# Performance work log

Measured on AMD Instinct MI355X. Metric: run time of the kernel, lower is better.

Reference implementation:

```python
import jax, jax.numpy as jnp
import numpy as np


def setup_inputs() -> dict:
    key = jax.random.key(0)
    k1, k2, k3 = jax.random.split(key, 3)
    N, D, V = 16384, 256, 8192
    return {
        "z_real": jax.random.normal(k1, (N, D), jnp.float32),
        "z_imag": jax.random.normal(k2, (N, D), jnp.float32),
        "weight": jax.random.normal(k3, (V, 2 * D), jnp.float32) / np.sqrt(2 * D).astype(np.float32),
    }


def reference(z_real, z_imag, weight):
    sg = jax.lax.stop_gradient
    N, D = z_real.shape
    V = weight.shape[0]
    z_flat = jnp.concatenate([z_real, z_imag], axis=-1)  # (N, 2D)
    # Squared euclidean distance expansion; argmin over squared dist == argmin over cdist.
    x2 = jnp.sum(z_flat * z_flat, axis=-1, keepdims=True)            # (N, 1)
    w2 = jnp.sum(weight * weight, axis=-1)                           # (V,)
    d2 = x2 + w2[None, :] - 2.0 * jnp.einsum('nd,vd->nv', z_flat, weight)  # (N, V)
    indices = jnp.argmin(d2, axis=-1)                                # (N,)
    z_q = weight[indices]                                            # (N, 2D)
    # codebook loss + 0.25 * commitment loss, per-sample mean over feature dim
    loss_sample = jnp.mean((z_q - sg(z_flat)) ** 2, axis=-1) \
                + 0.25 * jnp.mean((sg(z_q) - z_flat) ** 2, axis=-1)  # (N,)
    # straight-through estimator
    z_q_st = z_flat + sg(z_q - z_flat)                               # (N, 2D)
    # entropy of empirical code usage (equivalent to one_hot(indices).mean(0))
    counts = jnp.zeros((V,), z_flat.dtype).at[indices].add(1.0)
    avg_probs = counts / jnp.asarray(N, z_flat.dtype)
    entropy = -jnp.sum(avg_probs * jnp.log(avg_probs + 1e-10))
    # split straight-through output back into real / imag halves (complex output)
    return z_q_st[..., :D], z_q_st[..., D:], loss_sample, indices, entropy
```

## Files before the change

### kernel.cpp

```cpp
#include <hip/hip_runtime.h>
#include <cmath>

typedef _Float16 half8 __attribute__((ext_vector_type(8)));
typedef float f32x4 __attribute__((ext_vector_type(4)));

constexpr int N = 16384;
constexpr int D = 256;
constexpr int K = 512;
constexpr int V = 8192;
constexpr float TAU = 0.015f;

#define GLOAD16(g, l) __builtin_amdgcn_global_load_lds(                     \
    (const __attribute__((address_space(1))) void*)(g),                    \
    (__attribute__((address_space(3))) void*)(l), 16, 0, 0)

__global__ __launch_bounds__(256) void vq_cvt_z(
    const float* __restrict__ zr, const float* __restrict__ zi,
    _Float16* __restrict__ Zf) {
  int t = blockIdx.x * 256 + threadIdx.x;
  int n = t >> 6, c8 = t & 63, k = c8 * 8;
  const float* src = (k < D) ? zr + (size_t)n * D + k : zi + (size_t)n * D + (k - D);
  float4 a = *(const float4*)src;
  float4 b = *(const float4*)(src + 4);
  half8 h;
  h[0] = (_Float16)a.x; h[1] = (_Float16)a.y; h[2] = (_Float16)a.z; h[3] = (_Float16)a.w;
  h[4] = (_Float16)b.x; h[5] = (_Float16)b.y; h[6] = (_Float16)b.z; h[7] = (_Float16)b.w;
  *(half8*)&Zf[(size_t)n * K + k] = h;
}

__global__ __launch_bounds__(256) void vq_cvt_w(
    const float* __restrict__ w, _Float16* __restrict__ Wf) {
  int t = blockIdx.x * 256 + threadIdx.x;
  int vrow = t >> 6, c8 = t & 63, k = c8 * 8;
  const float* src = w + (size_t)vrow * K + k;
  float4 a = *(const float4*)src;
  float4 b = *(const float4*)(src + 4);
  half8 h;
  h[0] = (_Float16)a.x; h[1] = (_Float16)a.y; h[2] = (_Float16)a.z; h[3] = (_Float16)a.w;
  h[4] = (_Float16)b.x; h[5] = (_Float16)b.y; h[6] = (_Float16)b.z; h[7] = (_Float16)b.w;
  *(half8*)&Wf[(size_t)vrow * K + k] = h;
}

__global__ __launch_bounds__(256) void vq_w2(const float* __restrict__ w,
                                             double* __restrict__ w2d,
                                             float* __restrict__ w2f) {
  int v = blockIdx.x * 4 + (threadIdx.x >> 6);
  int lane = threadIdx.x & 63;
  const float4* wr = (const float4*)(w + (size_t)v * K);
  float4 a = wr[lane];
  float4 b = wr[64 + lane];
  double s = (double)a.x * a.x + (double)a.y * a.y + (double)a.z * a.z + (double)a.w * a.w +
             (double)b.x * b.x + (double)b.y * b.y + (double)b.z * b.z + (double)b.w * b.w;
#pragma unroll
  for (int off = 1; off < 64; off <<= 1) s += __shfl_xor(s, off, 64);
  if (lane == 0) { w2d[v] = s; w2f[v] = (float)s; }
}

__global__ __launch_bounds__(512, 2) void vq_pass1(
    const _Float16* __restrict__ Zf, const _Float16* __restrict__ Wf,
    const float* __restrict__ w2f,
    float* __restrict__ pm1, float* __restrict__ pm2, int* __restrict__ pi1) {
  __shared__ __align__(16) unsigned short smem[3][16384];

  const int tid = threadIdx.x;
  const int w = tid >> 6, lane = tid & 63;
  const int wr = w >> 2, wc = w & 3;
  const int tx = lane & 15, g = lane >> 4;
  const int rsub = lane >> 2, kq = lane & 3;
  const int vt = blockIdx.x & 31, nt = blockIdx.x >> 5;
  const int rowBase = nt * 256, colBase = vt * 256;

  f32x4 acc[8][4];
#pragma unroll
  for (int m = 0; m < 8; ++m)
#pragma unroll
    for (int n = 0; n < 4; ++n) acc[m][n] = f32x4{0.f, 0.f, 0.f, 0.f};

  const int sst = (rsub >> 1) & 3;
  const int srd = (tx >> 1) & 3;

  const int zc0 = 2 * w, zc1 = 2 * w + 1;
  const int row0 = zc0 * 16 + rsub, row1 = zc1 * 16 + rsub;
  const int klane = ((kq ^ sst) << 3);

  const _Float16* z0 = Zf + (size_t)(rowBase + row0) * K + klane;
  const _Float16* z1 = Zf + (size_t)(rowBase + row1) * K + klane;
  const _Float16* w0 = Wf + (size_t)(colBase + row0) * K + klane;
  const _Float16* w1 = Wf + (size_t)(colBase + row1) * K + klane;

#define STAGE(buf, koff)                                                      \
  do {                                                                        \
    GLOAD16(z0 + (koff), &smem[buf][zc0 * 512]);                              \
    GLOAD16(z1 + (koff), &smem[buf][zc1 * 512]);                              \
    GLOAD16(w0 + (koff), &smem[buf][8192 + zc0 * 512]);                       \
    GLOAD16(w1 + (koff), &smem[buf][8192 + zc1 * 512]);                       \
  } while (0)

  STAGE(0, 0);
  STAGE(1, 32);
  STAGE(2, 64);

#pragma unroll
  for (int t = 0; t < 16; ++t) {
    const int cur = t % 3;
    if (t <= 13)      asm volatile("s_waitcnt vmcnt(8)" ::: "memory");
    else if (t == 14) asm volatile("s_waitcnt vmcnt(4)" ::: "memory");
    else              asm volatile("s_waitcnt vmcnt(0)" ::: "memory");
    __builtin_amdgcn_s_barrier();

    half8 a[8], b[4];
#pragma unroll
    for (int m = 0; m < 8; ++m) {
      const int off = (wr * 128 + m * 16 + tx) * 32 + ((g ^ srd) << 3);
      a[m] = *(const half8*)&smem[cur][off];
    }
#pragma unroll
    for (int n = 0; n < 4; ++n) {
      const int off = 8192 + (wc * 64 + n * 16 + tx) * 32 + ((g ^ srd) << 3);
      b[n] = *(const half8*)&smem[cur][off];
    }
    __builtin_amdgcn_s_setprio(1);
#pragma unroll
    for (int m = 0; m < 8; ++m)
#pragma unroll
      for (int n = 0; n < 4; ++n)
        acc[m][n] = __builtin_amdgcn_mfma_f32_16x16x32_f16(a[m], b[n], acc[m][n], 0, 0, 0);
    __builtin_amdgcn_s_setprio(0);
    __builtin_amdgcn_s_barrier();
    if (t <= 12) STAGE(cur, (t + 3) * 32);
  }
#undef STAGE

  float wcol[4];
#pragma unroll
  for (int n = 0; n < 4; ++n) wcol[n] = w2f[colBase + wc * 64 + n * 16 + tx];
  const int cb = vt * 4 + wc;

#pragma unroll
  for (int m = 0; m < 8; ++m) {
#pragma unroll
    for (int r = 0; r < 4; ++r) {
      float m1 = 3.4e38f, m2 = 3.4e38f;
      int i1 = 0;
#pragma unroll
      for (int n = 0; n < 4; ++n) {
        float s = fmaf(-2.0f, acc[m][n][r], wcol[n]);
        if (s < m1) { m2 = m1; m1 = s; i1 = colBase + wc * 64 + n * 16 + tx; }
        else m2 = fminf(m2, s);
      }
#pragma unroll
      for (int off = 1; off < 16; off <<= 1) {
        float om1 = __shfl_xor(m1, off, 64);
        float om2 = __shfl_xor(m2, off, 64);
        int oi = __shfl_xor(i1, off, 64);
        float nm2 = fminf(fmaxf(m1, om1), fminf(m2, om2));
        if (om1 < m1 || (om1 == m1 && oi < i1)) { m1 = om1; i1 = oi; }
        m2 = nm2;
      }
      if (tx == 0) {
        int row = rowBase + wr * 128 + m * 16 + g * 4 + r;
        size_t o = (size_t)row * 128 + cb;
        pm1[o] = m1; pm2[o] = m2; pi1[o] = i1;
      }
    }
  }
}

__global__ __launch_bounds__(256) void vq_reduce(
    const float* __restrict__ pm1, const float* __restrict__ pm2,
    const int* __restrict__ pi1,
    float* __restrict__ out_idx, int* __restrict__ ws_idx,
    int* __restrict__ flaglist, int* __restrict__ nflag) {
  int row = blockIdx.x * 4 + (threadIdx.x >> 6);
  int lane = threadIdx.x & 63;
  size_t b = (size_t)row * 128;
  float a1 = pm1[b + lane], a2 = pm2[b + lane];
  int ai = pi1[b + lane];
  float b1 = pm1[b + lane + 64], b2 = pm2[b + lane + 64];
  int bi = pi1[b + lane + 64];
  float nm2 = fminf(fmaxf(a1, b1), fminf(a2, b2));
  if (b1 < a1 || (b1 == a1 && bi < ai)) { a1 = b1; ai = bi; }
  a2 = nm2;
#pragma unroll
  for (int off = 1; off < 64; off <<= 1) {
    float o1 = __shfl_xor(a1, off, 64);
    float o2 = __shfl_xor(a2, off, 64);
    int oi = __shfl_xor(ai, off, 64);
    float n2 = fminf(fmaxf(a1, o1), fminf(a2, o2));
    if (o1 < a1 || (o1 == a1 && oi < ai)) { a1 = o1; ai = oi; }
    a2 = n2;
  }
  if (lane == 0) {
    out_idx[row] = (float)ai;
    ws_idx[row] = ai;
    if (a2 - a1 < TAU) {
      int slot = atomicAdd(nflag, 1);
      flaglist[slot] = row;
    }
  }
}

__global__ __launch_bounds__(256) void vq_fixup(
    const float* __restrict__ zr, const float* __restrict__ zi,
    const float* __restrict__ w, const double* __restrict__ w2d,
    const float* __restrict__ pm1, const float* __restrict__ pm2,
    const int* __restrict__ pi1,
    const int* __restrict__ flaglist, const int* __restrict__ nflag,
    float* __restrict__ out_idx, int* __restrict__ ws_idx) {
  __shared__ float zrow[K];
  __shared__ float redf[128];
  __shared__ int slist[128];
  __shared__ int hlist[128];
  __shared__ int ns_s, nh_s;
  __shared__ float thr_s;
  __shared__ double wmin[4];
  __shared__ int widx[4];
  const int tid = threadIdx.x;
  const int lane = tid & 63, wvq = tid >> 6;
  const int nf = *nflag;

  for (int f = blockIdx.x; f < nf; f += gridDim.x) {
    const int row = flaglist[f];
    __syncthreads();
    if (tid == 0) { ns_s = 0; nh_s = 0; }
    zrow[tid] = zr[(size_t)row * D + tid];
    zrow[256 + tid] = zi[(size_t)row * D + tid];
    if (tid < 128) redf[tid] = pm1[(size_t)row * 128 + tid];
    __syncthreads();
    if (wvq == 0) {
      float v = fminf(redf[lane], redf[lane + 64]);
#pragma unroll
      for (int off = 1; off < 64; off <<= 1) v = fminf(v, __shfl_xor(v, off, 64));
      if (lane == 0) thr_s = v + TAU;
    }
    __syncthreads();
    const float thr = thr_s;
    if (tid < 128) {
      if (pm2[(size_t)row * 128 + tid] <= thr) {
        hlist[atomicAdd(&nh_s, 1)] = tid;
      } else if (redf[tid] <= thr) {
        slist[atomicAdd(&ns_s, 1)] = pi1[(size_t)row * 128 + tid];
      }
    }
    __syncthreads();
    const int ns = ns_s, nh = nh_s;

    double best = 1e300;
    int bi = 0x7fffffff;

    for (int ci = tid >> 3; ci < ns; ci += 32) {
      const int code = slist[ci], sub = tid & 7;
      const float4* w4 = (const float4*)(w + (size_t)code * K + sub * 64);
      const float4* z4 = (const float4*)(zrow + sub * 64);
      double d0 = 0.0, d1 = 0.0;
#pragma unroll
      for (int k4 = 0; k4 < 16; k4 += 2) {
        float4 a0 = w4[k4], b0 = z4[k4];
        float4 a1 = w4[k4 + 1], b1 = z4[k4 + 1];
        d0 = fma((double)a0.x, (double)b0.x, d0); d0 = fma((double)a0.y, (double)b0.y, d0);
        d0 = fma((double)a0.z, (double)b0.z, d0); d0 = fma((double)a0.w, (double)b0.w, d0);
        d1 = fma((double)a1.x, (double)b1.x, d1); d1 = fma((double)a1.y, (double)b1.y, d1);
        d1 = fma((double)a1.z, (double)b1.z, d1); d1 = fma((double)a1.w, (double)b1.w, d1);
      }
      double dot = d0 + d1;
      dot += __shfl_xor(dot, 1, 64);
      dot += __shfl_xor(dot, 2, 64);
      dot += __shfl_xor(dot, 4, 64);
      if (sub == 0) {
        double d = w2d[code] - 2.0 * dot;
        if (d < best || (d == best && code < bi)) { best = d; bi = code; }
      }
    }

    for (int hi = wvq; hi < nh; hi += 4) {
      const int code = hlist[hi] * 64 + lane;
      const float4* w4 = (const float4*)(w + (size_t)code * K);
      const float4* z4 = (const float4*)zrow;
      double d0 = 0.0, d1 = 0.0, d2 = 0.0, d3 = 0.0;
      for (int k4 = 0; k4 < 128; k4 += 4) {
        float4 a0 = w4[k4], b0 = z4[k4];
        float4 a1 = w4[k4 + 1], b1 = z4[k4 + 1];
        float4 a2 = w4[k4 + 2], b2 = z4[k4 + 2];
        float4 a3 = w4[k4 + 3], b3 = z4[k4 + 3];
        d0 = fma((double)a0.x, (double)b0.x, d0); d0 = fma((double)a0.y, (double)b0.y, d0);
        d0 = fma((double)a0.z, (double)b0.z, d0); d0 = fma((double)a0.w, (double)b0.w, d0);
        d1 = fma((double)a1.x, (double)b1.x, d1); d1 = fma((double)a1.y, (double)b1.y, d1);
        d1 = fma((double)a1.z, (double)b1.z, d1); d1 = fma((double)a1.w, (double)b1.w, d1);
        d2 = fma((double)a2.x, (double)b2.x, d2); d2 = fma((double)a2.y, (double)b2.y, d2);
        d2 = fma((double)a2.z, (double)b2.z, d2); d2 = fma((double)a2.w, (double)b2.w, d2);
        d3 = fma((double)a3.x, (double)b3.x, d3); d3 = fma((double)a3.y, (double)b3.y, d3);
        d3 = fma((double)a3.z, (double)b3.z, d3); d3 = fma((double)a3.w, (double)b3.w, d3);
      }
      double d = w2d[code] - 2.0 * ((d0 + d1) + (d2 + d3));
      if (d < best || (d == best && code < bi)) { best = d; bi = code; }
    }

#pragma unroll
    for (int off = 1; off < 64; off <<= 1) {
      double ob = __shfl_xor(best, off, 64);
      int oi = __shfl_xor(bi, off, 64);
      if (ob < best || (ob == best && oi < bi)) { best = ob; bi = oi; }
    }
    if (lane == 0) { wmin[wvq] = best; widx[wvq] = bi; }
    __syncthreads();
    if (tid == 0) {
      double b0 = wmin[0]; int i0 = widx[0];
      for (int q = 1; q < 4; ++q)
        if (wmin[q] < b0 || (wmin[q] == b0 && widx[q] < i0)) { b0 = wmin[q]; i0 = widx[q]; }
      out_idx[row] = (float)i0;
      ws_idx[row] = i0;
    }
  }
}

__global__ __launch_bounds__(256) void vq_gather(
    const float* __restrict__ zr, const float* __restrict__ zi,
    const float* __restrict__ w, const int* __restrict__ ws_idx,
    float* __restrict__ out0, float* __restrict__ out1,
    float* __restrict__ out2, unsigned int* __restrict__ counts) {
  int row = blockIdx.x * 4 + (threadIdx.x >> 6);
  int lane = threadIdx.x & 63;
  int idx = ws_idx[row];
  const float4* wr = (const float4*)(w + (size_t)idx * K);
  float4 q0 = wr[lane];
  float4 q1 = wr[64 + lane];
  float4 a = ((const float4*)(zr + (size_t)row * D))[lane];
  float4 b = ((const float4*)(zi + (size_t)row * D))[lane];
  ((float4*)(out0 + (size_t)row * D))[lane] = q0;
  ((float4*)(out1 + (size_t)row * D))[lane] = q1;

  float s = 0.f, dx;
  dx = q0.x - a.x; s = fmaf(dx, dx, s);
  dx = q0.y - a.y; s = fmaf(dx, dx, s);
  dx = q0.z - a.z; s = fmaf(dx, dx, s);
  dx = q0.w - a.w; s = fmaf(dx, dx, s);
  dx = q1.x - b.x; s = fmaf(dx, dx, s);
  dx = q1.y - b.y; s = fmaf(dx, dx, s);
  dx = q1.z - b.z; s = fmaf(dx, dx, s);
  dx = q1.w - b.w; s = fmaf(dx, dx, s);
#pragma unroll
  for (int off = 1; off < 64; off <<= 1) s += __shfl_xor(s, off, 64);
  if (lane == 0) {
    out2[row] = s * (1.25f / 512.f);
    atomicAdd(counts + idx, 1u);
  }
}

__global__ __launch_bounds__(256) void vq_entropy(const unsigned int* __restrict__ counts,
                                                  float* __restrict__ out4) {
  __shared__ double sd[256];
  int tid = threadIdx.x;
  double e = 0.0;
  for (int v = tid; v < V; v += 256) {
    double p = (double)counts[v] * (1.0 / (double)N);
    e += p * log(p + 1e-10);
  }
  sd[tid] = e;
  __syncthreads();
  for (int s = 128; s > 0; s >>= 1) {
    if (tid < s) sd[tid] += sd[tid + s];
    __syncthreads();
  }
  if (tid == 0) *out4 = -(float)sd[0];
}

extern "C" void kernel_launch(void* const* d_in, const int* in_sizes, int n_in,
                              void* d_out, int out_size, void* d_ws, size_t ws_size,
                              hipStream_t stream) {
  const float* zr = (const float*)d_in[0];
  const float* zi = (const float*)d_in[1];
  const float* w = (const float*)d_in[2];

  float* out = (float*)d_out;
  float* out0 = out;
  float* out1 = out + (size_t)N * D;
  float* out2 = out + (size_t)2 * N * D;
  float* out3 = out2 + N;
  float* out4 = out3 + N;

  float* pm1 = out;
  float* pm2 = out + (size_t)N * 128;
  int* pi1 = (int*)(out + (size_t)2 * N * 128);

  char* ws = (char*)d_ws;
  _Float16* Zf = (_Float16*)ws;
  _Float16* Wf = (_Float16*)(ws + (((size_t)16) << 20));
  char* ws2 = ws + (((size_t)24) << 20);
  double* w2d = (double*)ws2;
  float* w2f = (float*)(ws2 + 65536);
  unsigned int* counts = (unsigned int*)(ws2 + 98304);
  int* ws_idx = (int*)(ws2 + 131072);
  int* flaglist = (int*)(ws2 + 196608);
  int* nflag = (int*)(ws2 + 262144);

  (void)hipMemsetAsync(counts, 0, V * sizeof(unsigned int), stream);
  (void)hipMemsetAsync(nflag, 0, sizeof(int), stream);

  vq_cvt_z<<<N * 64 / 256, 256, 0, stream>>>(zr, zi, Zf);
  vq_cvt_w<<<V * 64 / 256, 256, 0, stream>>>(w, Wf);
  vq_w2<<<V / 4, 256, 0, stream>>>(w, w2d, w2f);
  vq_pass1<<<(N / 256) * (V / 256), 512, 0, stream>>>(Zf, Wf, w2f, pm1, pm2, pi1);
  vq_reduce<<<N / 4, 256, 0, stream>>>(pm1, pm2, pi1, out3, ws_idx, flaglist, nflag);
  vq_fixup<<<4096, 256, 0, stream>>>(zr, zi, w, w2d, pm1, pm2, pi1, flaglist, nflag,
                                     out3, ws_idx);
  vq_gather<<<N / 4, 256, 0, stream>>>(zr, zi, w, ws_idx, out0, out1, out2, counts);
  vq_entropy<<<1, 256, 0, stream>>>(counts, out4);
}
```

Measured before the change: 342.6 us.

## Restructure pass1 GEMM into 8-phase ping-pong schedule with 64-wide K tiles

Replaces the triple-buffered 32-wide K loop with a double-buffered 64-wide K tile. Each tile is split into four quarter phases that interleave LDS fragment reads, global-to-LDS prefetches and MFMA bursts, separated by barriers and explicit lgkmcnt waits. The LDS swizzle changes to an 8-way XOR on 128-byte rows. The aim is to hide load latency and LDS bank conflicts behind the matrix cores, at the cost of many more barriers per tile.

```diff
diff --git a/kernel.cpp b/kernel.cpp
--- a/kernel.cpp
+++ b/kernel.cpp
@@ -60,13 +60,13 @@
     const _Float16* __restrict__ Zf, const _Float16* __restrict__ Wf,
     const float* __restrict__ w2f,
     float* __restrict__ pm1, float* __restrict__ pm2, int* __restrict__ pi1) {
-  __shared__ __align__(16) unsigned short smem[3][16384];
+  __shared__ __align__(16) unsigned short smem[65536];
 
   const int tid = threadIdx.x;
   const int w = tid >> 6, lane = tid & 63;
   const int wr = w >> 2, wc = w & 3;
   const int tx = lane & 15, g = lane >> 4;
-  const int rsub = lane >> 2, kq = lane & 3;
+  const int rsub = lane >> 3, koct = lane & 7;
   const int vt = blockIdx.x & 31, nt = blockIdx.x >> 5;
   const int rowBase = nt * 256, colBase = vt * 256;
 
@@ -76,60 +76,104 @@
 #pragma unroll
     for (int n = 0; n < 4; ++n) acc[m][n] = f32x4{0.f, 0.f, 0.f, 0.f};
 
-  const int sst = (rsub >> 1) & 3;
-  const int srd = (tx >> 1) & 3;
-
-  const int zc0 = 2 * w, zc1 = 2 * w + 1;
-  const int row0 = zc0 * 16 + rsub, row1 = zc1 * 16 + rsub;
-  const int klane = ((kq ^ sst) << 3);
-
-  const _Float16* z0 = Zf + (size_t)(rowBase + row0) * K + klane;
-  const _Float16* z1 = Zf + (size_t)(rowBase + row1) * K + klane;
-  const _Float16* w0 = Wf + (size_t)(colBase + row0) * K + klane;
-  const _Float16* w1 = Wf + (size_t)(colBase + row1) * K + klane;
-
-#define STAGE(buf, koff)                                                      \
-  do {                                                                        \
-    GLOAD16(z0 + (koff), &smem[buf][zc0 * 512]);                              \
-    GLOAD16(z1 + (koff), &smem[buf][zc1 * 512]);                              \
-    GLOAD16(w0 + (koff), &smem[buf][8192 + zc0 * 512]);                       \
-    GLOAD16(w1 + (koff), &smem[buf][8192 + zc1 * 512]);                       \
+  const int swz = ((koct ^ rsub) << 3);
+  const _Float16* pZ = Zf + (size_t)(rowBase + 16 * w + rsub) * K + swz;
+  const _Float16* pW = Wf + (size_t)(colBase + 16 * w + rsub) * K + swz;
+  const int c0 = 2 * w, c1 = 2 * w + 1;
+
+#define STAGE_A(slot, half, kt) do {                                          \
+    GLOAD16(pZ + (half) * 128 * K + (kt) * 64,                                \
+            &smem[(slot) * 16384 + (half) * 8192 + c0 * 512]);                \
+    GLOAD16(pZ + 8 * K + (half) * 128 * K + (kt) * 64,                        \
+            &smem[(slot) * 16384 + (half) * 8192 + c1 * 512]);                \
   } while (0)
-
-  STAGE(0, 0);
-  STAGE(1, 32);
-  STAGE(2, 64);
-
-#pragma unroll
-  for (int t = 0; t < 16; ++t) {
-    const int cur = t % 3;
-    if (t <= 13)      asm volatile("s_waitcnt vmcnt(8)" ::: "memory");
-    else if (t == 14) asm volatile("s_waitcnt vmcnt(4)" ::: "memory");
-    else              asm volatile("s_waitcnt vmcnt(0)" ::: "memory");
-    __builtin_amdgcn_s_barrier();
-
-    half8 a[8], b[4];
-#pragma unroll
-    for (int m = 0; m < 8; ++m) {
-      const int off = (wr * 128 + m * 16 + tx) * 32 + ((g ^ srd) << 3);
-      a[m] = *(const half8*)&smem[cur][off];
-    }
-#pragma unroll
-    for (int n = 0; n < 4; ++n) {
-      const int off = 8192 + (wc * 64 + n * 16 + tx) * 32 + ((g ^ srd) << 3);
-      b[n] = *(const half8*)&smem[cur][off];
-    }
+#define STAGE_B(slot, half, kt) do {                                          \
+    GLOAD16(pW + (half) * 128 * K + (kt) * 64,                                \
+            &smem[32768 + (slot) * 16384 + (half) * 8192 + c0 * 512]);        \
+    GLOAD16(pW + 8 * K + (half) * 128 * K + (kt) * 64,                        \
+            &smem[32768 + (slot) * 16384 + (half) * 8192 + c1 * 512]);        \
+  } while (0)
+
+  half8 afr[2][2], bfr[4][2];
+  auto rdA = [&](int slot, int q) {
+#pragma unroll
+    for (int mi = 0; mi < 2; ++mi)
+#pragma unroll
+      for (int ks = 0; ks < 2; ++ks) {
+        const int r = (q * 2 + mi) * 16 + tx;
+        const int oct = (ks * 4 + g) ^ (tx & 7);
+        afr[mi][ks] = *(const half8*)&smem[slot * 16384 + wr * 8192 + r * 64 + oct * 8];
+      }
+  };
+  auto rdB = [&](int slot) {
+#pragma unroll
+    for (int n = 0; n < 4; ++n)
+#pragma unroll
+      for (int ks = 0; ks < 2; ++ks) {
+        const int c = wc * 64 + n * 16 + tx;
+        const int oct = (ks * 4 + g) ^ (tx & 7);
+        bfr[n][ks] = *(const half8*)&smem[32768 + slot * 16384 + (c >> 7) * 8192 +
+                                          (c & 127) * 64 + oct * 8];
+      }
+  };
+  auto mm = [&](int q) {
     __builtin_amdgcn_s_setprio(1);
 #pragma unroll
-    for (int m = 0; m < 8; ++m)
-#pragma unroll
-      for (int n = 0; n < 4; ++n)
-        acc[m][n] = __builtin_amdgcn_mfma_f32_16x16x32_f16(a[m], b[n], acc[m][n], 0, 0, 0);
+    for (int mi = 0; mi < 2; ++mi)
+#pragma unroll
+      for (int n = 0; n < 4; ++n) {
+        acc[q * 2 + mi][n] =
+            __builtin_amdgcn_mfma_f32_16x16x32_f16(afr[mi][0], bfr[n][0], acc[q * 2 + mi][n], 0, 0, 0);
+        acc[q * 2 + mi][n] =
+            __builtin_amdgcn_mfma_f32_16x16x32_f16(afr[mi][1], bfr[n][1], acc[q * 2 + mi][n], 0, 0, 0);
+      }
     __builtin_amdgcn_s_setprio(0);
-    __builtin_amdgcn_s_barrier();
-    if (t <= 12) STAGE(cur, (t + 3) * 32);
-  }
-#undef STAGE
+  };
+#define BAR() __builtin_amdgcn_s_barrier()
+#define LGKM0() do { asm volatile("s_waitcnt lgkmcnt(0)" ::: "memory");       \
+                     __builtin_amdgcn_sched_barrier(0); } while (0)
+
+  STAGE_A(0, 0, 0); STAGE_A(0, 1, 0); STAGE_B(0, 0, 0); STAGE_B(0, 1, 0);
+  STAGE_B(1, 0, 1); STAGE_B(1, 1, 1);
+  asm volatile("s_waitcnt vmcnt(4)" ::: "memory");
+  BAR();
+
+#pragma unroll
+  for (int i = 0; i < 4; ++i) {
+    const int kb = 2 * i + 1, ka2 = 2 * i + 2, kb2 = 2 * i + 3;
+    rdA(0, 0); rdB(0);
+    STAGE_A(1, 0, kb);
+    BAR(); LGKM0(); mm(0); BAR();
+    rdA(0, 1);
+    STAGE_A(1, 1, kb);
+    BAR(); LGKM0(); mm(1); BAR();
+    rdA(0, 2);
+    if (i < 3) STAGE_B(0, 0, ka2);
+    BAR(); LGKM0(); mm(2); BAR();
+    rdA(0, 3);
+    if (i < 3) STAGE_B(0, 1, ka2);
+    if (i < 3) asm volatile("s_waitcnt vmcnt(4)" ::: "memory");
+    else       asm volatile("s_waitcnt vmcnt(0)" ::: "memory");
+    BAR(); LGKM0(); mm(3); BAR();
+    rdA(1, 0); rdB(1);
+    if (i < 3) STAGE_A(0, 0, ka2);
+    BAR(); LGKM0(); mm(0); BAR();
+    rdA(1, 1);
+    if (i < 3) STAGE_A(0, 1, ka2);
+    BAR(); LGKM0(); mm(1); BAR();
+    rdA(1, 2);
+    if (i < 3) STAGE_B(1, 0, kb2);
+    BAR(); LGKM0(); mm(2); BAR();
+    rdA(1, 3);
+    if (i < 3) STAGE_B(1, 1, kb2);
+    if (i < 3) asm volatile("s_waitcnt vmcnt(4)" ::: "memory");
+    else       asm volatile("s_waitcnt vmcnt(0)" ::: "memory");
+    BAR(); LGKM0(); mm(3); BAR();
+  }
+#undef STAGE_A
+#undef STAGE_B
+#undef BAR
+#undef LGKM0
 
   float wcol[4];
 #pragma unroll
```

Measured after the change: 335.2 us. 1.02x faster.
